# Kernel optimization log

Hardware: AMD Instinct MI355X
Metric: run time of the kernel (lower is better)

## Reference

```python
import jax, jax.numpy as jnp
import numpy as np

N_HEAD = 16
N_FEAT = 1024
D_K = N_FEAT // N_HEAD


def setup_inputs() -> dict:
    key = jax.random.key(0)
    ks = jax.random.split(key, 12)
    B, T, F = 4, 2048, N_FEAT
    s = 1.0 / np.sqrt(F)
    return {
        "query": jax.random.normal(ks[0], (B, T, F), dtype=jnp.float32),
        "key": jax.random.normal(ks[1], (B, T, F), dtype=jnp.float32),
        "value": jax.random.normal(ks[2], (B, T, F), dtype=jnp.float32),
        "mask": jnp.ones((B, 1, T), dtype=jnp.int32),
        "Wq": jax.random.normal(ks[3], (F, F), dtype=jnp.float32) * s,
        "bq": jax.random.normal(ks[4], (F,), dtype=jnp.float32) * 0.01,
        "Wk": jax.random.normal(ks[5], (F, F), dtype=jnp.float32) * s,
        "bk": jax.random.normal(ks[6], (F,), dtype=jnp.float32) * 0.01,
        "Wv": jax.random.normal(ks[7], (F, F), dtype=jnp.float32) * s,
        "bv": jax.random.normal(ks[8], (F,), dtype=jnp.float32) * 0.01,
        "Wo": jax.random.normal(ks[9], (F, F), dtype=jnp.float32) * s,
        "bo": jax.random.normal(ks[10], (F,), dtype=jnp.float32) * 0.01,
    }


def reference(query, key, value, mask, Wq, bq, Wk, bk, Wv, bv, Wo, bo):
    B, Tq, F = query.shape
    Tk = key.shape[1]
    h, dk = N_HEAD, D_K
    # torch nn.Linear: y = x @ W.T + b ; then view [B,T,h,dk] and transpose to [B,h,T,dk]
    q = (query @ Wq.T + bq).reshape(B, Tq, h, dk).transpose(0, 2, 1, 3)
    k = (key @ Wk.T + bk).reshape(B, Tk, h, dk).transpose(0, 2, 1, 3)
    v = (value @ Wv.T + bv).reshape(B, Tk, h, dk).transpose(0, 2, 1, 3)
    scale = 1.0 / np.sqrt(dk).astype(np.float32)
    scores = jnp.einsum("bhqd,bhkd->bhqk", q, k) * scale  # [B,h,Tq,Tk]
    # mask [B,1,Tk] -> unsqueeze(1) -> [B,1,1,Tk], True where mask == 0 (padded)
    pad = (mask[:, None, :, :] == 0)
    min_value = jnp.finfo(scores.dtype).min
    scores = jnp.where(pad, min_value, scores)
    atten = jax.nn.softmax(scores, axis=-1)
    atten = jnp.where(pad, 0.0, atten)
    # dropout_rate = 0.0 (eval): identity
    x = jnp.einsum("bhqk,bhkd->bhqd", atten, v)  # [B,h,Tq,dk]
    x = x.transpose(0, 2, 1, 3).reshape(B, Tq, h * dk)
    return x @ Wo.T + bo
```

## Files before the change

### kernel.cpp

```cpp
#include <hip/hip_runtime.h>
#include <hip/hip_bf16.h>


typedef unsigned short u16;
typedef unsigned long long u64;
typedef __attribute__((ext_vector_type(8))) short short8;
typedef __attribute__((ext_vector_type(4))) float f32x4;
typedef __attribute__((ext_vector_type(16))) float f32x16;
typedef __attribute__((ext_vector_type(4))) unsigned int u32x4;

#define GLOAD16(g, l) __builtin_amdgcn_global_load_lds( \
    (const __attribute__((address_space(1))) unsigned int*)(g), \
    (__attribute__((address_space(3))) unsigned int*)(l), 16, 0, 0)

__device__ __forceinline__ u16 f2bf(float x) {
  unsigned int u = __float_as_uint(x);
  return (u16)((u + 0x7fffu + ((u >> 16) & 1u)) >> 16);
}

__device__ __forceinline__ float fexp2(float x) {
#if __has_builtin(__builtin_amdgcn_exp2f)
  return __builtin_amdgcn_exp2f(x);
#else
  return exp2f(x);
#endif
}

__device__ __forceinline__ unsigned cvtpk(float lo, float hi) {
  unsigned r;
  asm("v_cvt_pk_bf16_f32 %0, %1, %2" : "=v"(r) : "v"(lo), "v"(hi));
  return r;
}

struct CvtArgs {
  const float* src[4];
  u16* dst[4];
};

__global__ __launch_bounds__(256) void cvt_multi(CvtArgs a, int shift) {
  const int id = blockIdx.x * 256 + threadIdx.x;
  const int seg = id >> shift;
  const int off = id & ((1 << shift) - 1);
  float4 v = ((const float4*)a.src[seg])[off];
  ushort4 o;
  o.x = f2bf(v.x); o.y = f2bf(v.y); o.z = f2bf(v.z); o.w = f2bf(v.w);
  ((ushort4*)a.dst[seg])[off] = o;
}

template <int EPI>
__global__ __launch_bounds__(256) void gemm_bt(const u16* __restrict__ A,
                                               const u16* __restrict__ Bw,
                                               const float* __restrict__ bias,
                                               void* __restrict__ Cout,
                                               float scale) {
  __shared__ u16 As[128 * 64];
  __shared__ u16 Bs[128 * 64];
  const int t = threadIdx.x;
  const int lane = t & 63;
  const int w = t >> 6;
  const int wm = w >> 1, wn = w & 1;
  const int l15 = lane & 15, l4 = lane >> 4;

  const int bid = blockIdx.x;
  const int swz = (bid & 7) * 64 + (bid >> 3);
  const int brow = swz >> 3;
  const int bcol = swz & 7;

  f32x4 acc[4][4] = {};

  const int srow = t >> 3;
  const int sbyte = (t & 7) * 16;

  for (int kt = 0; kt < 16; ++kt) {
    const int k0 = kt * 64;
    __syncthreads();
#pragma unroll
    for (int i = 0; i < 4; ++i) {
      const int r = i * 32 + srow;
      const int sb = sbyte ^ ((r & 7) << 4);
      GLOAD16((const char*)(A + (size_t)(brow * 128 + r) * 1024 + k0) + sb,
              &As[(i * 4096 + t * 16) >> 1]);
      GLOAD16((const char*)(Bw + (size_t)(bcol * 128 + r) * 1024 + k0) + sb,
              &Bs[(i * 4096 + t * 16) >> 1]);
    }
    __syncthreads();
#pragma unroll
    for (int kf = 0; kf < 2; ++kf) {
      short8 af[4], bfv[4];
#pragma unroll
      for (int mi = 0; mi < 4; ++mi) {
        const int r = wm * 64 + mi * 16 + l15;
        const int byt = r * 128 + ((kf * 64 + l4 * 16) ^ ((r & 7) << 4));
        af[mi] = *(const short8*)&As[byt >> 1];
      }
#pragma unroll
      for (int ni = 0; ni < 4; ++ni) {
        const int r = wn * 64 + ni * 16 + l15;
        const int byt = r * 128 + ((kf * 64 + l4 * 16) ^ ((r & 7) << 4));
        bfv[ni] = *(const short8*)&Bs[byt >> 1];
      }
#pragma unroll
      for (int mi = 0; mi < 4; ++mi)
#pragma unroll
        for (int ni = 0; ni < 4; ++ni)
          acc[mi][ni] = __builtin_amdgcn_mfma_f32_16x16x32_bf16(
              af[mi], bfv[ni], acc[mi][ni], 0, 0, 0);
    }
  }

#pragma unroll
  for (int ni = 0; ni < 4; ++ni) {
    const int n = bcol * 128 + wn * 64 + ni * 16 + l15;
    const float bn = bias[n];
#pragma unroll
    for (int mi = 0; mi < 4; ++mi) {
      const int mb = brow * 128 + wm * 64 + mi * 16 + l4 * 4;
#pragma unroll
      for (int r = 0; r < 4; ++r) {
        const float v = acc[mi][ni][r] + bn;
        const int m = mb + r;
        const int b_ = m >> 11, tok = m & 2047, h_ = n >> 6, d = n & 63;
        if (EPI == 0) {
          ((u16*)Cout)[(((size_t)(b_ * 16 + h_) * 2048 + tok) << 6) + d] = f2bf(v * scale);
        } else if (EPI == 2) {
          ((u16*)Cout)[(((size_t)(b_ * 16 + h_) * 64 + d) << 11) + tok] = f2bf(v);
        } else {
          ((float*)Cout)[(size_t)m * 1024 + n] = v;
        }
      }
    }
  }
}

__global__ __launch_bounds__(256, 2) void attn_fwd5(const u16* __restrict__ Q,
                                                    const u16* __restrict__ Kp,
                                                    const u16* __restrict__ Vt,
                                                    const int* __restrict__ mask,
                                                    u16* __restrict__ ctx) {
  __shared__ u16 Ks[2][64 * 64];
  __shared__ u16 Vs[2][64 * 64];

  const int t = threadIdx.x, lane = t & 63, w = t >> 6;
  const int q31 = lane & 31, hi = lane >> 5;

  const int bid = blockIdx.x;
  const int swz = (bid & 7) * 64 + (bid >> 3);
  const int bh = swz >> 3;
  const int b_ = bh >> 4, h_ = bh & 15;
  const int q0 = (swz & 7) * 256 + w * 64;
  const size_t headO = (size_t)bh * 131072;

  short8 qfA[4], qfB[4];
  {
    const u16* qrowA = Q + headO + (size_t)(q0 + q31) * 64 + hi * 8;
    const u16* qrowB = qrowA + 32 * 64;
#pragma unroll
    for (int ds = 0; ds < 4; ++ds) {
      qfA[ds] = *(const short8*)(qrowA + ds * 16);
      qfB[ds] = *(const short8*)(qrowB + ds * 16);
    }
  }

  const int srow = t >> 3;
  const int sbyte = (t & 7) * 16;

#define STAGE_KV(bufi, kb)                                                      \
  {                                                                             \
    _Pragma("unroll") for (int i = 0; i < 2; ++i) {                             \
      const int r = i * 32 + srow;                                              \
      const int sb = sbyte ^ ((r & 7) << 4);                                    \
      GLOAD16((const char*)(Kp + headO + (size_t)((kb) + r) * 64) + sb,         \
              &Ks[bufi][(i * 4096 + t * 16) >> 1]);                             \
      GLOAD16((const char*)(Vt + headO + (size_t)r * 2048 + (kb)) + sb,         \
              &Vs[bufi][(i * 4096 + t * 16) >> 1]);                             \
    }                                                                           \
  }

#define PACK(sv, pfa, pfb)                                                      \
  {                                                                             \
    const unsigned w0 = cvtpk(sv[0], sv[1]),   w1 = cvtpk(sv[2], sv[3]);        \
    const unsigned w2 = cvtpk(sv[4], sv[5]),   w3 = cvtpk(sv[6], sv[7]);        \
    const unsigned w4 = cvtpk(sv[8], sv[9]),   w5 = cvtpk(sv[10], sv[11]);      \
    const unsigned w6 = cvtpk(sv[12], sv[13]), w7 = cvtpk(sv[14], sv[15]);      \
    const unsigned x0 = (unsigned)__shfl_xor((int)(hi ? w0 : w2), 32);          \
    const unsigned x1 = (unsigned)__shfl_xor((int)(hi ? w1 : w3), 32);          \
    const unsigned y0 = (unsigned)__shfl_xor((int)(hi ? w4 : w6), 32);          \
    const unsigned y1 = (unsigned)__shfl_xor((int)(hi ? w5 : w7), 32);          \
    u32x4 fa = hi ? (u32x4){x0, x1, w2, w3} : (u32x4){w0, w1, x0, x1};          \
    u32x4 fb = hi ? (u32x4){y0, y1, w6, w7} : (u32x4){w4, w5, y0, y1};          \
    pfa = __builtin_bit_cast(short8, fa);                                       \
    pfb = __builtin_bit_cast(short8, fb);                                       \
  }

  f32x16 oA0 = {}, oA1 = {}, oB0 = {}, oB1 = {};
  float lA = 0.f, lB = 0.f;
  const int kcol = hi * 16;
  const int rswz = (q31 & 7) << 4;

  STAGE_KV(0, 0);
  int mk = mask[b_ * 2048 + lane];
  __syncthreads();

  int buf = 0;
  for (int kt = 0; kt < 32; ++kt) {
    const int kb = kt * 64;
    if (kt + 1 < 32) STAGE_KV(buf ^ 1, kb + 64);
    const int mk_next = (kt + 1 < 32) ? mask[b_ * 2048 + kb + 64 + lane] : 0;
    const u64 bits = __ballot(mk != 0);

#pragma unroll
    for (int half = 0; half < 2; ++half) {
      f32x16 sA = {}, sB = {};
      __builtin_amdgcn_s_setprio(1);
#pragma unroll
      for (int ds = 0; ds < 4; ++ds) {
        const int byt = (half * 32 + q31) * 128 + ((ds * 32 + kcol) ^ rswz);
        short8 ka = *(const short8*)&Ks[buf][byt >> 1];
        sA = __builtin_amdgcn_mfma_f32_32x32x16_bf16(ka, qfA[ds], sA, 0, 0, 0);
        sB = __builtin_amdgcn_mfma_f32_32x32x16_bf16(ka, qfB[ds], sB, 0, 0, 0);
      }
      __builtin_amdgcn_s_setprio(0);

      if (bits == ~0ull) {
#pragma unroll
        for (int r = 0; r < 16; ++r) { sA[r] = fexp2(sA[r]); sB[r] = fexp2(sB[r]); }
      } else {
#pragma unroll
        for (int r = 0; r < 16; ++r) {
          const int k0 = half * 32 + (r & 3) + 8 * (r >> 2) + 4 * hi;
          const bool on = (bits >> k0) & 1;
          sA[r] = on ? fexp2(sA[r]) : 0.f;
          sB[r] = on ? fexp2(sB[r]) : 0.f;
        }
      }

      {
        float a0 = 0.f, a1 = 0.f, b0 = 0.f, b1 = 0.f;
#pragma unroll
        for (int r = 0; r < 16; r += 2) {
          a0 += sA[r]; a1 += sA[r + 1];
          b0 += sB[r]; b1 += sB[r + 1];
        }
        lA += a0 + a1;
        lB += b0 + b1;
      }

      short8 pA0, pA1, pB0, pB1;
      PACK(sA, pA0, pA1);
      PACK(sB, pB0, pB1);

      __builtin_amdgcn_s_setprio(1);
      {
        const int rb0 = q31 * 128, rb1 = (32 + q31) * 128;
        const int c0 = (half * 64 + kcol) ^ rswz;
        const int c1 = (half * 64 + 32 + kcol) ^ rswz;
        short8 va;
        va = *(const short8*)&Vs[buf][(rb0 + c0) >> 1];
        oA0 = __builtin_amdgcn_mfma_f32_32x32x16_bf16(va, pA0, oA0, 0, 0, 0);
        oB0 = __builtin_amdgcn_mfma_f32_32x32x16_bf16(va, pB0, oB0, 0, 0, 0);
        va = *(const short8*)&Vs[buf][(rb0 + c1) >> 1];
        oA0 = __builtin_amdgcn_mfma_f32_32x32x16_bf16(va, pA1, oA0, 0, 0, 0);
        oB0 = __builtin_amdgcn_mfma_f32_32x32x16_bf16(va, pB1, oB0, 0, 0, 0);
        va = *(const short8*)&Vs[buf][(rb1 + c0) >> 1];
        oA1 = __builtin_amdgcn_mfma_f32_32x32x16_bf16(va, pA0, oA1, 0, 0, 0);
        oB1 = __builtin_amdgcn_mfma_f32_32x32x16_bf16(va, pB0, oB1, 0, 0, 0);
        va = *(const short8*)&Vs[buf][(rb1 + c1) >> 1];
        oA1 = __builtin_amdgcn_mfma_f32_32x32x16_bf16(va, pA1, oA1, 0, 0, 0);
        oB1 = __builtin_amdgcn_mfma_f32_32x32x16_bf16(va, pB1, oB1, 0, 0, 0);
      }
      __builtin_amdgcn_s_setprio(0);
    }

    mk = mk_next;
    __syncthreads();
    buf ^= 1;
  }
#undef STAGE_KV

  lA += __shfl_xor(lA, 32);
  lB += __shfl_xor(lB, 32);
  const float invA = lA > 0.f ? 1.f / lA : 0.f;
  const float invB = lB > 0.f ? 1.f / lB : 0.f;
  const int tokA = q0 + q31;
  u16* crowA = ctx + ((size_t)b_ * 2048 + tokA) * 1024 + h_ * 64 + 4 * hi;
  u16* crowB = crowA + 32 * 1024;
#pragma unroll
  for (int g = 0; g < 4; ++g) {
    unsigned u0, u1;
    u0 = cvtpk(oA0[4 * g + 0] * invA, oA0[4 * g + 1] * invA);
    u1 = cvtpk(oA0[4 * g + 2] * invA, oA0[4 * g + 3] * invA);
    *(uint2*)(crowA + 8 * g) = make_uint2(u0, u1);
    u0 = cvtpk(oA1[4 * g + 0] * invA, oA1[4 * g + 1] * invA);
    u1 = cvtpk(oA1[4 * g + 2] * invA, oA1[4 * g + 3] * invA);
    *(uint2*)(crowA + 32 + 8 * g) = make_uint2(u0, u1);
    u0 = cvtpk(oB0[4 * g + 0] * invB, oB0[4 * g + 1] * invB);
    u1 = cvtpk(oB0[4 * g + 2] * invB, oB0[4 * g + 3] * invB);
    *(uint2*)(crowB + 8 * g) = make_uint2(u0, u1);
    u0 = cvtpk(oB1[4 * g + 0] * invB, oB1[4 * g + 1] * invB);
    u1 = cvtpk(oB1[4 * g + 2] * invB, oB1[4 * g + 3] * invB);
    *(uint2*)(crowB + 32 + 8 * g) = make_uint2(u0, u1);
  }
}

extern "C" void kernel_launch(void* const* d_in, const int* in_sizes, int n_in,
                              void* d_out, int out_size, void* d_ws, size_t ws_size,
                              hipStream_t stream) {
  const float* q_in = (const float*)d_in[0];
  const float* k_in = (const float*)d_in[1];
  const float* v_in = (const float*)d_in[2];
  const int*   mask = (const int*)d_in[3];
  const float* Wq = (const float*)d_in[4];
  const float* bq = (const float*)d_in[5];
  const float* Wk = (const float*)d_in[6];
  const float* bk = (const float*)d_in[7];
  const float* Wv = (const float*)d_in[8];
  const float* bv = (const float*)d_in[9];
  const float* Wo = (const float*)d_in[10];
  const float* bo = (const float*)d_in[11];
  float* out = (float*)d_out;

  char* ws = (char*)d_ws;
  u16* xq = (u16*)(ws);
  u16* xk = (u16*)(ws + 16777216);
  u16* xv = (u16*)(ws + 33554432);
  u16* Qp = (u16*)(ws + 50331648);
  u16* Kp = (u16*)(ws + 67108864);
  u16* Vtb = (u16*)(ws + 83886080);
  u16* wqb = (u16*)(ws + 100663296);
  u16* wkb = (u16*)(ws + 102760448);
  u16* wvb = (u16*)(ws + 104857600);
  u16* wob = (u16*)(ws + 106954752);
  u16* ctx = xk;

  CvtArgs big;
  big.src[0] = q_in; big.src[1] = k_in; big.src[2] = v_in; big.src[3] = v_in;
  big.dst[0] = xq;   big.dst[1] = xk;   big.dst[2] = xv;   big.dst[3] = xv;
  cvt_multi<<<3 * 8192, 256, 0, stream>>>(big, 21);
  CvtArgs wts;
  wts.src[0] = Wq;  wts.src[1] = Wk;  wts.src[2] = Wv;  wts.src[3] = Wo;
  wts.dst[0] = wqb; wts.dst[1] = wkb; wts.dst[2] = wvb; wts.dst[3] = wob;
  cvt_multi<<<4 * 1024, 256, 0, stream>>>(wts, 18);

  const float C_SCALE = 0.18033688011112042f;
  gemm_bt<0><<<512, 256, 0, stream>>>(xq, wqb, bq, Qp, C_SCALE);
  gemm_bt<0><<<512, 256, 0, stream>>>(xk, wkb, bk, Kp, 1.0f);
  gemm_bt<2><<<512, 256, 0, stream>>>(xv, wvb, bv, Vtb, 1.0f);

  attn_fwd5<<<512, 256, 0, stream>>>(Qp, Kp, Vtb, mask, ctx);

  gemm_bt<1><<<512, 256, 0, stream>>>(ctx, wob, bo, out, 1.0f);
}
```

Measured before the change: 227.5 us.

## Split attention key range across two wave groups and reduce partial outputs in LDS

The attention kernel now launches 512 threads per block, and two groups of four waves each process half of the key sequence for the same query rows. Each group stages its own double-buffered K/V tiles into a 64 KB shared buffer. At the end, the partial output accumulators and row sums are combined through shared memory in two rounds before normalisation and the store. This doubles the waves available per CU to hide latency in a 512-block grid, at the cost of more LDS, extra synchronisation and a reduction step.

```diff
diff --git a/kernel.cpp b/kernel.cpp
--- a/kernel.cpp
+++ b/kernel.cpp
@@ -132,22 +132,23 @@
   }
 }
 
-__global__ __launch_bounds__(256, 2) void attn_fwd5(const u16* __restrict__ Q,
+__global__ __launch_bounds__(512, 4) void attn_fwd6(const u16* __restrict__ Q,
                                                     const u16* __restrict__ Kp,
                                                     const u16* __restrict__ Vt,
                                                     const int* __restrict__ mask,
                                                     u16* __restrict__ ctx) {
-  __shared__ u16 Ks[2][64 * 64];
-  __shared__ u16 Vs[2][64 * 64];
+  __shared__ __align__(16) char smem[65536];
 
   const int t = threadIdx.x, lane = t & 63, w = t >> 6;
   const int q31 = lane & 31, hi = lane >> 5;
+  const int khalf = w >> 2;
+  const int koff = khalf << 10;
 
   const int bid = blockIdx.x;
   const int swz = (bid & 7) * 64 + (bid >> 3);
   const int bh = swz >> 3;
   const int b_ = bh >> 4, h_ = bh & 15;
-  const int q0 = (swz & 7) * 256 + w * 64;
+  const int q0 = (swz & 7) * 256 + (w & 3) * 64;
   const size_t headO = (size_t)bh * 131072;
 
   short8 qfA[4], qfB[4];
@@ -161,19 +162,22 @@
     }
   }
 
-  const int srow = t >> 3;
-  const int sbyte = (t & 7) * 16;
-
-#define STAGE_KV(bufi, kb)                                                      \
-  {                                                                             \
-    _Pragma("unroll") for (int i = 0; i < 2; ++i) {                             \
-      const int r = i * 32 + srow;                                              \
-      const int sb = sbyte ^ ((r & 7) << 4);                                    \
-      GLOAD16((const char*)(Kp + headO + (size_t)((kb) + r) * 64) + sb,         \
-              &Ks[bufi][(i * 4096 + t * 16) >> 1]);                             \
-      GLOAD16((const char*)(Vt + headO + (size_t)r * 2048 + (kb)) + sb,         \
-              &Vs[bufi][(i * 4096 + t * 16) >> 1]);                             \
-    }                                                                           \
+  const int tl = t & 255;
+  const int srow = tl >> 3;
+  const int sbyte = (tl & 7) * 16;
+
+#define STAGE_KV(bufi, kb)                                                        \
+  {                                                                               \
+    char* kdst = smem + (khalf << 14) + ((bufi) << 13) + tl * 16;                 \
+    char* vdst = smem + 32768 + (khalf << 14) + ((bufi) << 13) + tl * 16;         \
+    _Pragma("unroll") for (int i = 0; i < 2; ++i) {                               \
+      const int r = i * 32 + srow;                                                \
+      const int sb = sbyte ^ ((r & 7) << 4);                                      \
+      GLOAD16((const char*)(Kp + headO + (size_t)(koff + (kb) + r) * 64) + sb,    \
+              (u16*)(kdst + i * 4096));                                           \
+      GLOAD16((const char*)(Vt + headO + (size_t)r * 2048 + koff + (kb)) + sb,    \
+              (u16*)(vdst + i * 4096));                                           \
+    }                                                                             \
   }
 
 #define PACK(sv, pfa, pfb)                                                      \
@@ -198,15 +202,18 @@
   const int rswz = (q31 & 7) << 4;
 
   STAGE_KV(0, 0);
-  int mk = mask[b_ * 2048 + lane];
+  int mk = mask[b_ * 2048 + koff + lane];
   __syncthreads();
 
   int buf = 0;
-  for (int kt = 0; kt < 32; ++kt) {
+  for (int kt = 0; kt < 16; ++kt) {
     const int kb = kt * 64;
-    if (kt + 1 < 32) STAGE_KV(buf ^ 1, kb + 64);
-    const int mk_next = (kt + 1 < 32) ? mask[b_ * 2048 + kb + 64 + lane] : 0;
+    if (kt + 1 < 16) STAGE_KV(buf ^ 1, kb + 64);
+    const int mk_next = (kt + 1 < 16) ? mask[b_ * 2048 + koff + kb + 64 + lane] : 0;
     const u64 bits = __ballot(mk != 0);
+
+    const char* kc = smem + (khalf << 14) + (buf << 13);
+    const char* vc = kc + 32768;
 
 #pragma unroll
     for (int half = 0; half < 2; ++half) {
@@ -215,7 +222,7 @@
 #pragma unroll
       for (int ds = 0; ds < 4; ++ds) {
         const int byt = (half * 32 + q31) * 128 + ((ds * 32 + kcol) ^ rswz);
-        short8 ka = *(const short8*)&Ks[buf][byt >> 1];
+        short8 ka = *(const short8*)(kc + byt);
         sA = __builtin_amdgcn_mfma_f32_32x32x16_bf16(ka, qfA[ds], sA, 0, 0, 0);
         sB = __builtin_amdgcn_mfma_f32_32x32x16_bf16(ka, qfB[ds], sB, 0, 0, 0);
       }
@@ -255,16 +262,16 @@
         const int c0 = (half * 64 + kcol) ^ rswz;
         const int c1 = (half * 64 + 32 + kcol) ^ rswz;
         short8 va;
-        va = *(const short8*)&Vs[buf][(rb0 + c0) >> 1];
+        va = *(const short8*)(vc + rb0 + c0);
         oA0 = __builtin_amdgcn_mfma_f32_32x32x16_bf16(va, pA0, oA0, 0, 0, 0);
         oB0 = __builtin_amdgcn_mfma_f32_32x32x16_bf16(va, pB0, oB0, 0, 0, 0);
-        va = *(const short8*)&Vs[buf][(rb0 + c1) >> 1];
+        va = *(const short8*)(vc + rb0 + c1);
         oA0 = __builtin_amdgcn_mfma_f32_32x32x16_bf16(va, pA1, oA0, 0, 0, 0);
         oB0 = __builtin_amdgcn_mfma_f32_32x32x16_bf16(va, pB1, oB0, 0, 0, 0);
-        va = *(const short8*)&Vs[buf][(rb1 + c0) >> 1];
+        va = *(const short8*)(vc + rb1 + c0);
         oA1 = __builtin_amdgcn_mfma_f32_32x32x16_bf16(va, pA0, oA1, 0, 0, 0);
         oB1 = __builtin_amdgcn_mfma_f32_32x32x16_bf16(va, pB0, oB1, 0, 0, 0);
-        va = *(const short8*)&Vs[buf][(rb1 + c1) >> 1];
+        va = *(const short8*)(vc + rb1 + c1);
         oA1 = __builtin_amdgcn_mfma_f32_32x32x16_bf16(va, pA1, oA1, 0, 0, 0);
         oB1 = __builtin_amdgcn_mfma_f32_32x32x16_bf16(va, pB1, oB1, 0, 0, 0);
       }
@@ -277,28 +284,62 @@
   }
 #undef STAGE_KV
 
-  lA += __shfl_xor(lA, 32);
-  lB += __shfl_xor(lB, 32);
-  const float invA = lA > 0.f ? 1.f / lA : 0.f;
-  const float invB = lB > 0.f ? 1.f / lB : 0.f;
-  const int tokA = q0 + q31;
-  u16* crowA = ctx + ((size_t)b_ * 2048 + tokA) * 1024 + h_ * 64 + 4 * hi;
-  u16* crowB = crowA + 32 * 1024;
-#pragma unroll
-  for (int g = 0; g < 4; ++g) {
-    unsigned u0, u1;
-    u0 = cvtpk(oA0[4 * g + 0] * invA, oA0[4 * g + 1] * invA);
-    u1 = cvtpk(oA0[4 * g + 2] * invA, oA0[4 * g + 3] * invA);
-    *(uint2*)(crowA + 8 * g) = make_uint2(u0, u1);
-    u0 = cvtpk(oA1[4 * g + 0] * invA, oA1[4 * g + 1] * invA);
-    u1 = cvtpk(oA1[4 * g + 2] * invA, oA1[4 * g + 3] * invA);
-    *(uint2*)(crowA + 32 + 8 * g) = make_uint2(u0, u1);
-    u0 = cvtpk(oB0[4 * g + 0] * invB, oB0[4 * g + 1] * invB);
-    u1 = cvtpk(oB0[4 * g + 2] * invB, oB0[4 * g + 3] * invB);
-    *(uint2*)(crowB + 8 * g) = make_uint2(u0, u1);
-    u0 = cvtpk(oB1[4 * g + 0] * invB, oB1[4 * g + 1] * invB);
-    u1 = cvtpk(oB1[4 * g + 2] * invB, oB1[4 * g + 3] * invB);
-    *(uint2*)(crowB + 32 + 8 * g) = make_uint2(u0, u1);
+  float* comb = (float*)smem;
+#pragma unroll
+  for (int rnd = 0; rnd < 2; ++rnd) {
+    if ((w >> 1) == 2 + rnd) {
+      float* dst = comb + ((w & 1) * 64 + lane) * 68;
+      float4* d4 = (float4*)dst;
+#pragma unroll
+      for (int g = 0; g < 4; ++g) {
+        d4[g]      = make_float4(oA0[4*g], oA0[4*g+1], oA0[4*g+2], oA0[4*g+3]);
+        d4[4 + g]  = make_float4(oA1[4*g], oA1[4*g+1], oA1[4*g+2], oA1[4*g+3]);
+        d4[8 + g]  = make_float4(oB0[4*g], oB0[4*g+1], oB0[4*g+2], oB0[4*g+3]);
+        d4[12 + g] = make_float4(oB1[4*g], oB1[4*g+1], oB1[4*g+2], oB1[4*g+3]);
+      }
+      dst[64] = lA; dst[65] = lB;
+    }
+    __syncthreads();
+    if ((w >> 1) == rnd) {
+      const float* src = comb + ((w & 1) * 64 + lane) * 68;
+      const float4* s4 = (const float4*)src;
+#pragma unroll
+      for (int g = 0; g < 4; ++g) {
+        float4 x;
+        x = s4[g];      oA0[4*g] += x.x; oA0[4*g+1] += x.y; oA0[4*g+2] += x.z; oA0[4*g+3] += x.w;
+        x = s4[4 + g];  oA1[4*g] += x.x; oA1[4*g+1] += x.y; oA1[4*g+2] += x.z; oA1[4*g+3] += x.w;
+        x = s4[8 + g];  oB0[4*g] += x.x; oB0[4*g+1] += x.y; oB0[4*g+2] += x.z; oB0[4*g+3] += x.w;
+        x = s4[12 + g]; oB1[4*g] += x.x; oB1[4*g+1] += x.y; oB1[4*g+2] += x.z; oB1[4*g+3] += x.w;
+      }
+      lA += src[64]; lB += src[65];
+    }
+    __syncthreads();
+  }
+
+  if (w < 4) {
+    lA += __shfl_xor(lA, 32);
+    lB += __shfl_xor(lB, 32);
+    const float invA = lA > 0.f ? 1.f / lA : 0.f;
+    const float invB = lB > 0.f ? 1.f / lB : 0.f;
+    const int tokA = q0 + q31;
+    u16* crowA = ctx + ((size_t)b_ * 2048 + tokA) * 1024 + h_ * 64 + 4 * hi;
+    u16* crowB = crowA + 32 * 1024;
+#pragma unroll
+    for (int g = 0; g < 4; ++g) {
+      unsigned u0, u1;
+      u0 = cvtpk(oA0[4 * g + 0] * invA, oA0[4 * g + 1] * invA);
+      u1 = cvtpk(oA0[4 * g + 2] * invA, oA0[4 * g + 3] * invA);
+      *(uint2*)(crowA + 8 * g) = make_uint2(u0, u1);
+      u0 = cvtpk(oA1[4 * g + 0] * invA, oA1[4 * g + 1] * invA);
+      u1 = cvtpk(oA1[4 * g + 2] * invA, oA1[4 * g + 3] * invA);
+      *(uint2*)(crowA + 32 + 8 * g) = make_uint2(u0, u1);
+      u0 = cvtpk(oB0[4 * g + 0] * invB, oB0[4 * g + 1] * invB);
+      u1 = cvtpk(oB0[4 * g + 2] * invB, oB0[4 * g + 3] * invB);
+      *(uint2*)(crowB + 8 * g) = make_uint2(u0, u1);
+      u0 = cvtpk(oB1[4 * g + 0] * invB, oB1[4 * g + 1] * invB);
+      u1 = cvtpk(oB1[4 * g + 2] * invB, oB1[4 * g + 3] * invB);
+      *(uint2*)(crowB + 32 + 8 * g) = make_uint2(u0, u1);
+    }
   }
 }
 
@@ -346,7 +387,7 @@
   gemm_bt<0><<<512, 256, 0, stream>>>(xk, wkb, bk, Kp, 1.0f);
   gemm_bt<2><<<512, 256, 0, stream>>>(xv, wvb, bv, Vtb, 1.0f);
 
-  attn_fwd5<<<512, 256, 0, stream>>>(Qp, Kp, Vtb, mask, ctx);
+  attn_fwd6<<<512, 512, 0, stream>>>(Qp, Kp, Vtb, mask, ctx);
 
   gemm_bt<1><<<512, 256, 0, stream>>>(ctx, wob, bo, out, 1.0f);
 }
```

Measured after the change: 827.8 us. +263.9%, slower.

## Replace double-buffered LDS async loads with register-prefetched single-buffer staging

Applied to the files above, without the earlier changes.

The attention kernel no longer copies K/V tiles straight from global memory into a double-buffered LDS area. It now prefetches the next tile into registers, writes them into a single LDS buffer at the top of each iteration, and uses two barriers per iteration. This halves the LDS footprint and moves the wait on global loads off the barrier path. In exchange it uses more VGPRs and adds a second barrier per tile.

```diff
diff --git a/kernel.cpp b/kernel.cpp
--- a/kernel.cpp
+++ b/kernel.cpp
@@ -132,13 +132,13 @@
   }
 }
 
-__global__ __launch_bounds__(256, 2) void attn_fwd5(const u16* __restrict__ Q,
+__global__ __launch_bounds__(256, 2) void attn_fwd7(const u16* __restrict__ Q,
                                                     const u16* __restrict__ Kp,
                                                     const u16* __restrict__ Vt,
                                                     const int* __restrict__ mask,
                                                     u16* __restrict__ ctx) {
-  __shared__ u16 Ks[2][64 * 64];
-  __shared__ u16 Vs[2][64 * 64];
+  __shared__ u16 Ks[64 * 64];
+  __shared__ u16 Vs[64 * 64];
 
   const int t = threadIdx.x, lane = t & 63, w = t >> 6;
   const int q31 = lane & 31, hi = lane >> 5;
@@ -163,17 +163,22 @@
 
   const int srow = t >> 3;
   const int sbyte = (t & 7) * 16;
-
-#define STAGE_KV(bufi, kb)                                                      \
-  {                                                                             \
-    _Pragma("unroll") for (int i = 0; i < 2; ++i) {                             \
-      const int r = i * 32 + srow;                                              \
-      const int sb = sbyte ^ ((r & 7) << 4);                                    \
-      GLOAD16((const char*)(Kp + headO + (size_t)((kb) + r) * 64) + sb,         \
-              &Ks[bufi][(i * 4096 + t * 16) >> 1]);                             \
-      GLOAD16((const char*)(Vt + headO + (size_t)r * 2048 + (kb)) + sb,         \
-              &Vs[bufi][(i * 4096 + t * 16) >> 1]);                             \
-    }                                                                           \
+  int lofs[2];
+#pragma unroll
+  for (int i = 0; i < 2; ++i) {
+    const int r = i * 32 + srow;
+    lofs[i] = r * 128 + (sbyte ^ ((r & 7) << 4));
+  }
+  const char* kgb = (const char*)(Kp + headO) + (size_t)srow * 128 + sbyte;
+  const char* vgb = (const char*)(Vt + headO) + (size_t)srow * 4096 + sbyte;
+
+  uint4 kr[2], vr[2];
+#define LOADT(kb)                                                   \
+  {                                                                 \
+    kr[0] = *(const uint4*)(kgb + (size_t)(kb) * 128);              \
+    kr[1] = *(const uint4*)(kgb + (size_t)(kb) * 128 + 4096);       \
+    vr[0] = *(const uint4*)(vgb + (size_t)(kb) * 2);                \
+    vr[1] = *(const uint4*)(vgb + (size_t)(kb) * 2 + 131072);       \
   }
 
 #define PACK(sv, pfa, pfb)                                                      \
@@ -197,15 +202,30 @@
   const int kcol = hi * 16;
   const int rswz = (q31 & 7) << 4;
 
-  STAGE_KV(0, 0);
   int mk = mask[b_ * 2048 + lane];
-  __syncthreads();
-
-  int buf = 0;
+  LOADT(0);
+  int mk_next;
+
   for (int kt = 0; kt < 32; ++kt) {
     const int kb = kt * 64;
-    if (kt + 1 < 32) STAGE_KV(buf ^ 1, kb + 64);
-    const int mk_next = (kt + 1 < 32) ? mask[b_ * 2048 + kb + 64 + lane] : 0;
+
+    *(uint4*)((char*)Ks + lofs[0]) = kr[0];
+    *(uint4*)((char*)Ks + lofs[1]) = kr[1];
+    *(uint4*)((char*)Vs + lofs[0]) = vr[0];
+    *(uint4*)((char*)Vs + lofs[1]) = vr[1];
+
+    if (kt < 31) {
+      mk_next = mask[b_ * 2048 + kb + 64 + lane];
+      LOADT(kb + 64);
+    } else {
+      mk_next = 0;
+    }
+
+    asm volatile("s_waitcnt lgkmcnt(0)" ::: "memory");
+    __builtin_amdgcn_sched_barrier(0);
+    __builtin_amdgcn_s_barrier();
+    __builtin_amdgcn_sched_barrier(0);
+
     const u64 bits = __ballot(mk != 0);
 
 #pragma unroll
@@ -215,7 +235,7 @@
 #pragma unroll
       for (int ds = 0; ds < 4; ++ds) {
         const int byt = (half * 32 + q31) * 128 + ((ds * 32 + kcol) ^ rswz);
-        short8 ka = *(const short8*)&Ks[buf][byt >> 1];
+        short8 ka = *(const short8*)((const char*)Ks + byt);
         sA = __builtin_amdgcn_mfma_f32_32x32x16_bf16(ka, qfA[ds], sA, 0, 0, 0);
         sB = __builtin_amdgcn_mfma_f32_32x32x16_bf16(ka, qfB[ds], sB, 0, 0, 0);
       }
@@ -255,27 +275,28 @@
         const int c0 = (half * 64 + kcol) ^ rswz;
         const int c1 = (half * 64 + 32 + kcol) ^ rswz;
         short8 va;
-        va = *(const short8*)&Vs[buf][(rb0 + c0) >> 1];
+        va = *(const short8*)((const char*)Vs + rb0 + c0);
         oA0 = __builtin_amdgcn_mfma_f32_32x32x16_bf16(va, pA0, oA0, 0, 0, 0);
         oB0 = __builtin_amdgcn_mfma_f32_32x32x16_bf16(va, pB0, oB0, 0, 0, 0);
-        va = *(const short8*)&Vs[buf][(rb0 + c1) >> 1];
+        va = *(const short8*)((const char*)Vs + rb0 + c1);
         oA0 = __builtin_amdgcn_mfma_f32_32x32x16_bf16(va, pA1, oA0, 0, 0, 0);
         oB0 = __builtin_amdgcn_mfma_f32_32x32x16_bf16(va, pB1, oB0, 0, 0, 0);
-        va = *(const short8*)&Vs[buf][(rb1 + c0) >> 1];
+        va = *(const short8*)((const char*)Vs + rb1 + c0);
         oA1 = __builtin_amdgcn_mfma_f32_32x32x16_bf16(va, pA0, oA1, 0, 0, 0);
         oB1 = __builtin_amdgcn_mfma_f32_32x32x16_bf16(va, pB0, oB1, 0, 0, 0);
-        va = *(const short8*)&Vs[buf][(rb1 + c1) >> 1];
+        va = *(const short8*)((const char*)Vs + rb1 + c1);
         oA1 = __builtin_amdgcn_mfma_f32_32x32x16_bf16(va, pA1, oA1, 0, 0, 0);
         oB1 = __builtin_amdgcn_mfma_f32_32x32x16_bf16(va, pB1, oB1, 0, 0, 0);
       }
       __builtin_amdgcn_s_setprio(0);
     }
 
+    __builtin_amdgcn_sched_barrier(0);
+    __builtin_amdgcn_s_barrier();
+    __builtin_amdgcn_sched_barrier(0);
     mk = mk_next;
-    __syncthreads();
-    buf ^= 1;
-  }
-#undef STAGE_KV
+  }
+#undef LOADT
 
   lA += __shfl_xor(lA, 32);
   lB += __shfl_xor(lB, 32);
@@ -346,7 +367,7 @@
   gemm_bt<0><<<512, 256, 0, stream>>>(xk, wkb, bk, Kp, 1.0f);
   gemm_bt<2><<<512, 256, 0, stream>>>(xv, wvb, bv, Vtb, 1.0f);
 
-  attn_fwd5<<<512, 256, 0, stream>>>(Qp, Kp, Vtb, mask, ctx);
+  attn_fwd7<<<512, 256, 0, stream>>>(Qp, Kp, Vtb, mask, ctx);
 
   gemm_bt<1><<<512, 256, 0, stream>>>(ctx, wob, bo, out, 1.0f);
 }
```

Measured after the change: 240.2 us. 5.6% more time.

## Fuse fp32-to-bf16 activation conversion into projection GEMM A-tile loads

Applied to the files above, without the earlier changes.

Drops the separate conversion kernel for query/key/value and has the Q/K/V projection GEMMs load fp32 activations straight into a doubled LDS tile, converting to bf16 at fragment read time. This removes a full read of 3x32MB fp32 plus a write and reread of 3x16MB bf16 intermediates, and one kernel launch. In exchange each GEMM reads twice the A bytes from global memory, uses twice the A-tile LDS, and does extra conversion ALU work in the inner loop, which may lower occupancy.

```diff
diff --git a/kernel.cpp b/kernel.cpp
--- a/kernel.cpp
+++ b/kernel.cpp
@@ -47,14 +47,14 @@
   ((ushort4*)a.dst[seg])[off] = o;
 }
 
-template <int EPI>
-__global__ __launch_bounds__(256) void gemm_bt(const u16* __restrict__ A,
+template <int EPI, int AF32>
+__global__ __launch_bounds__(256) void gemm_bt(const void* __restrict__ Ap,
                                                const u16* __restrict__ Bw,
                                                const float* __restrict__ bias,
                                                void* __restrict__ Cout,
                                                float scale) {
-  __shared__ u16 As[128 * 64];
-  __shared__ u16 Bs[128 * 64];
+  __shared__ __align__(16) char As[AF32 ? 32768 : 16384];
+  __shared__ __align__(16) char Bs[16384];
   const int t = threadIdx.x;
   const int lane = t & 63;
   const int w = t >> 6;
@@ -70,18 +70,37 @@
 
   const int srow = t >> 3;
   const int sbyte = (t & 7) * 16;
+  const int srowA = t >> 4;
+  const int sbyteA = (t & 15) * 16;
 
   for (int kt = 0; kt < 16; ++kt) {
     const int k0 = kt * 64;
     __syncthreads();
+    if constexpr (AF32) {
+      const float* A = (const float*)Ap;
+#pragma unroll
+      for (int i = 0; i < 8; ++i) {
+        const int r = i * 16 + srowA;
+        const int sb = sbyteA ^ ((r & 15) << 4);
+        GLOAD16((const char*)(A + (size_t)(brow * 128 + r) * 1024 + k0) + sb,
+                As + i * 4096 + t * 16);
+      }
+    } else {
+      const u16* A = (const u16*)Ap;
+#pragma unroll
+      for (int i = 0; i < 4; ++i) {
+        const int r = i * 32 + srow;
+        const int sb = sbyte ^ ((r & 7) << 4);
+        GLOAD16((const char*)(A + (size_t)(brow * 128 + r) * 1024 + k0) + sb,
+                As + i * 4096 + t * 16);
+      }
+    }
 #pragma unroll
     for (int i = 0; i < 4; ++i) {
       const int r = i * 32 + srow;
       const int sb = sbyte ^ ((r & 7) << 4);
-      GLOAD16((const char*)(A + (size_t)(brow * 128 + r) * 1024 + k0) + sb,
-              &As[(i * 4096 + t * 16) >> 1]);
       GLOAD16((const char*)(Bw + (size_t)(bcol * 128 + r) * 1024 + k0) + sb,
-              &Bs[(i * 4096 + t * 16) >> 1]);
+              Bs + i * 4096 + t * 16);
     }
     __syncthreads();
 #pragma unroll
@@ -90,14 +109,25 @@
 #pragma unroll
       for (int mi = 0; mi < 4; ++mi) {
         const int r = wm * 64 + mi * 16 + l15;
-        const int byt = r * 128 + ((kf * 64 + l4 * 16) ^ ((r & 7) << 4));
-        af[mi] = *(const short8*)&As[byt >> 1];
+        if constexpr (AF32) {
+          const int base = r * 256;
+          const int cb = kf * 128 + l4 * 32;
+          const int m0 = (r & 15) << 4;
+          float4 x = *(const float4*)(As + base + ((cb) ^ m0));
+          float4 y = *(const float4*)(As + base + ((cb + 16) ^ m0));
+          u32x4 p = {cvtpk(x.x, x.y), cvtpk(x.z, x.w),
+                     cvtpk(y.x, y.y), cvtpk(y.z, y.w)};
+          af[mi] = __builtin_bit_cast(short8, p);
+        } else {
+          const int byt = r * 128 + ((kf * 64 + l4 * 16) ^ ((r & 7) << 4));
+          af[mi] = *(const short8*)(As + byt);
+        }
       }
 #pragma unroll
       for (int ni = 0; ni < 4; ++ni) {
         const int r = wn * 64 + ni * 16 + l15;
         const int byt = r * 128 + ((kf * 64 + l4 * 16) ^ ((r & 7) << 4));
-        bfv[ni] = *(const short8*)&Bs[byt >> 1];
+        bfv[ni] = *(const short8*)(Bs + byt);
       }
 #pragma unroll
       for (int mi = 0; mi < 4; ++mi)
@@ -320,9 +350,7 @@
   float* out = (float*)d_out;
 
   char* ws = (char*)d_ws;
-  u16* xq = (u16*)(ws);
-  u16* xk = (u16*)(ws + 16777216);
-  u16* xv = (u16*)(ws + 33554432);
+  u16* ctx = (u16*)(ws);
   u16* Qp = (u16*)(ws + 50331648);
   u16* Kp = (u16*)(ws + 67108864);
   u16* Vtb = (u16*)(ws + 83886080);
@@ -330,23 +358,18 @@
   u16* wkb = (u16*)(ws + 102760448);
   u16* wvb = (u16*)(ws + 104857600);
   u16* wob = (u16*)(ws + 106954752);
-  u16* ctx = xk;
-
-  CvtArgs big;
-  big.src[0] = q_in; big.src[1] = k_in; big.src[2] = v_in; big.src[3] = v_in;
-  big.dst[0] = xq;   big.dst[1] = xk;   big.dst[2] = xv;   big.dst[3] = xv;
-  cvt_multi<<<3 * 8192, 256, 0, stream>>>(big, 21);
+
   CvtArgs wts;
   wts.src[0] = Wq;  wts.src[1] = Wk;  wts.src[2] = Wv;  wts.src[3] = Wo;
   wts.dst[0] = wqb; wts.dst[1] = wkb; wts.dst[2] = wvb; wts.dst[3] = wob;
   cvt_multi<<<4 * 1024, 256, 0, stream>>>(wts, 18);
 
   const float C_SCALE = 0.18033688011112042f;
-  gemm_bt<0><<<512, 256, 0, stream>>>(xq, wqb, bq, Qp, C_SCALE);
-  gemm_bt<0><<<512, 256, 0, stream>>>(xk, wkb, bk, Kp, 1.0f);
-  gemm_bt<2><<<512, 256, 0, stream>>>(xv, wvb, bv, Vtb, 1.0f);
+  gemm_bt<0, 1><<<512, 256, 0, stream>>>(q_in, wqb, bq, Qp, C_SCALE);
+  gemm_bt<0, 1><<<512, 256, 0, stream>>>(k_in, wkb, bk, Kp, 1.0f);
+  gemm_bt<2, 1><<<512, 256, 0, stream>>>(v_in, wvb, bv, Vtb, 1.0f);
 
   attn_fwd5<<<512, 256, 0, stream>>>(Qp, Kp, Vtb, mask, ctx);
 
-  gemm_bt<1><<<512, 256, 0, stream>>>(ctx, wob, bo, out, 1.0f);
-}
+  gemm_bt<1, 0><<<512, 256, 0, stream>>>(ctx, wob, bo, out, 1.0f);
+}
```

Measured after the change: 215.1 us. 1.06x faster.
